# Optimization experiments

Measured on AMD Instinct MI355X. Metric: run time of the kernel, lower is better.

Reference implementation:

```python
import jax, jax.numpy as jnp
import numpy as np

NUM_HIGH = 3
CHANNELS = 3

def _gauss_kernel(channels):
    k = jnp.array([[1., 4., 6., 4., 1.],
                   [4., 16., 24., 16., 4.],
                   [6., 24., 36., 24., 6.],
                   [4., 16., 24., 16., 4.],
                   [1., 4., 6., 4., 1.]], dtype=jnp.float32) / 256.0
    # depthwise kernel layout OIHW with I=1, O=channels
    return jnp.broadcast_to(k, (channels, 1, 5, 5))

def conv_gauss(img, kernel):
    # reflect-pad by 2 on H,W then depthwise (grouped) 5x5 conv, VALID
    p = jnp.pad(img, ((0, 0), (0, 0), (2, 2), (2, 2)), mode='reflect')
    return jax.lax.conv_general_dilated(
        p, kernel, window_strides=(1, 1), padding='VALID',
        feature_group_count=img.shape[1],
        dimension_numbers=('NCHW', 'OIHW', 'NCHW'))

def downsample(x):
    return x[:, :, ::2, ::2]

def upsample(x, kernel):
    B, C, H, W = x.shape
    x_up = jnp.zeros((B, C, 2 * H, 2 * W), dtype=x.dtype).at[:, :, ::2, ::2].set(x)
    return conv_gauss(x_up, 4.0 * kernel)

def setup_inputs() -> dict:
    key = jax.random.key(0)
    img = jax.random.normal(key, (8, CHANNELS, 1024, 1024), dtype=jnp.float32)
    kernel = _gauss_kernel(CHANNELS)
    return {"img": img, "kernel": kernel}

def reference(img, kernel):
    # pyramid_decom: Laplacian pyramid (H,W divisible by 2**NUM_HIGH, so no interpolate)
    current = img
    pyr = []
    for _ in range(NUM_HIGH):
        filtered = conv_gauss(current, kernel)
        down = downsample(filtered)
        up = upsample(down, kernel)
        pyr.append(current - up)
        current = down
    pyr.append(current)
    return tuple(pyr)
```

## Files before the change

### kernel.cpp

```cpp
#include <hip/hip_runtime.h>


__device__ __forceinline__ int refl(int t, int n) {
    if (t < 0) t = -t;
    if (t >= n) t = 2 * (n - 1) - t;
    return t;
}

__global__ __launch_bounds__(256, 6) void lap_scan_kernel(
    const float* __restrict__ cur, float* __restrict__ lap,
    float* __restrict__ down, int H, int W, int sh)
{
    const int wid = threadIdx.x >> 6, lane = threadIdx.x & 63;
    const int x0 = blockIdx.x * 128;
    const int y0 = (blockIdx.y * 4 + wid) * sh;
    const int img = blockIdx.z;
    const int Hh = H >> 1, Wh = W >> 1;

    const float* curb = cur + (size_t)img * H * W;
    float* lapb = lap + (size_t)img * H * W;
    float* downb = down + (size_t)img * Hh * Wh;

    const int c0 = x0 + 2 * lane;
    const bool haloLane = (lane < 2) | (lane >= 62);
    const int hc0 = (lane < 2) ? (x0 - 4 + 2 * lane) : (x0 + 4 + 2 * lane);
    const bool xb = (x0 == 0) || (x0 + 128 == W);
    const int hg0 = refl(hc0, W), hg1 = refl(hc0 + 1, W);

    auto loadOwn = [&](int rho) -> float2 {
        return *(const float2*)(curb + (size_t)refl(y0 + rho, H) * W + c0);
    };
    auto loadHalo = [&](int rho) -> float2 {
        const float* rp = curb + (size_t)refl(y0 + rho, H) * W;
        float2 v;
        if (xb) { v.x = rp[hg0]; v.y = rp[hg1]; }
        else    { v = *(const float2*)(rp + hc0); }
        return v;
    };

    float2 w0 = loadOwn(-4), w1 = loadOwn(-3), w2 = loadOwn(-2),
           w3 = loadOwn(-1), w4 = loadOwn(0);
    float2 h0 = {0,0}, h1 = {0,0}, h2 = {0,0}, h3 = {0,0}, h4 = {0,0};
    if (haloLane) {
        h0 = loadHalo(-4); h1 = loadHalo(-3); h2 = loadHalo(-2);
        h3 = loadHalo(-1); h4 = loadHalo(0);
    }

    float dm2a = 0, dm2b = 0, dm2c = 0, dm1a = 0, dm1b = 0, dm1c = 0;
    const int aEnd = sh >> 1;

    for (int a = -1; a <= aEnd; ++a) {
        float2 nw3 = {0,0}, nw4 = {0,0}, nh3 = {0,0}, nh4 = {0,0};
        const bool more = (a < aEnd);
        if (more) {
            nw3 = loadOwn(2 * a + 3); nw4 = loadOwn(2 * a + 4);
            if (haloLane) { nh3 = loadHalo(2 * a + 3); nh4 = loadHalo(2 * a + 4); }
        }

        float vE = w0.x + 4.f * w1.x + 6.f * w2.x + 4.f * w3.x + w4.x;
        float vO = w0.y + 4.f * w1.y + 6.f * w2.y + 4.f * w3.y + w4.y;
        float hE = h0.x + 4.f * h1.x + 6.f * h2.x + 4.f * h3.x + h4.x;
        float hO = h0.y + 4.f * h1.y + 6.f * h2.y + 4.f * h3.y + h4.y;

        float bhE0 = __shfl(hE, 0),  bhO0 = __shfl(hO, 0);
        float bhE1 = __shfl(hE, 1),  bhO1 = __shfl(hO, 1);
        float bhE62 = __shfl(hE, 62), bhO62 = __shfl(hO, 62);
        float bhE63 = __shfl(hE, 63);
        float bvE0 = __shfl(vE, 0);
        float bvE63 = __shfl(vE, 63), bvO63 = __shfl(vO, 63);

        float sE = __shfl_up(vE, 1), sO = __shfl_up(vO, 1);
        float nE = __shfl_down(vE, 1);
        float eL = (lane == 0) ? bhE1 : sE;
        float oL = (lane == 0) ? bhO1 : sO;
        float eR = (lane == 63) ? bhE62 : nE;

        float dv = (eL + 4.f * oL + 6.f * vE + 4.f * vO + eR) * (1.f / 256.f);
        float dvm1 = (bhE0 + 4.f * bhO0 + 6.f * bhE1 + 4.f * bhO1 + bvE0) * (1.f / 256.f);
        float dvp64 = (bvE63 + 4.f * bvO63 + 6.f * bhE62 + 4.f * bhO62 + bhE63) * (1.f / 256.f);

        float su = __shfl_up(dv, 1), sd = __shfl_down(dv, 1);
        float da = (lane == 0) ? dvm1 : su;
        float db = dv;
        float dc = (lane == 63) ? dvp64 : sd;

        if (a >= 0 && a < aEnd)
            downb[(size_t)((y0 >> 1) + a) * Wh + (x0 >> 1) + lane] = dv;

        if (a >= 1) {
            float CEa = dm2a + 6.f * dm1a + da;
            float CEb = dm2b + 6.f * dm1b + db;
            float CEc = dm2c + 6.f * dm1c + dc;
            float COa = 4.f * (dm1a + da);
            float COb = 4.f * (dm1b + db);
            float COc = 4.f * (dm1c + dc);
            float2 oe, oo;
            oe.x = w0.x - (CEa + 6.f * CEb + CEc) * (1.f / 64.f);
            oe.y = w0.y - 4.f * (CEb + CEc) * (1.f / 64.f);
            oo.x = w1.x - (COa + 6.f * COb + COc) * (1.f / 64.f);
            oo.y = w1.y - 4.f * (COb + COc) * (1.f / 64.f);
            *(float2*)(lapb + (size_t)(y0 + 2 * a - 2) * W + c0) = oe;
            *(float2*)(lapb + (size_t)(y0 + 2 * a - 1) * W + c0) = oo;
        }

        dm2a = dm1a; dm2b = dm1b; dm2c = dm1c;
        dm1a = da;   dm1b = db;   dm1c = dc;
        w0 = w2; w1 = w3; w2 = w4;
        if (more) { w3 = nw3; w4 = nw4; }
        h0 = h2; h1 = h3; h2 = h4;
        if (more) { h3 = nh3; h4 = nh4; }
    }
}

extern "C" void kernel_launch(void* const* d_in, const int* in_sizes, int n_in,
                              void* d_out, int out_size, void* d_ws, size_t ws_size,
                              hipStream_t stream) {
    const float* img = (const float*)d_in[0];
    float* out = (float*)d_out;

    const long long BC = 8LL * 3;
    const long long n0 = BC * 1024 * 1024;
    const long long n1 = BC * 512 * 512;
    const long long n2 = BC * 256 * 256;

    float* out0 = out;
    float* out1 = out0 + n0;
    float* out2 = out1 + n1;
    float* out3 = out2 + n2;

    float* ws0 = (float*)d_ws;
    float* ws1 = ws0 + n1;

    lap_scan_kernel<<<dim3(1024 / 128, 1024 / (4 * 32), (int)BC), 256, 0, stream>>>(
        img, out0, ws0, 1024, 1024, 32);
    lap_scan_kernel<<<dim3(512 / 128, 512 / (4 * 16), (int)BC), 256, 0, stream>>>(
        ws0, out1, ws1, 512, 512, 16);
    lap_scan_kernel<<<dim3(256 / 128, 256 / (4 * 8), (int)BC), 256, 0, stream>>>(
        ws1, out2, out3, 256, 256, 8);
}
```

Before: 71.80 us.

## Widen per-lane tile to four columns with float4 loads and fewer halo shuffles

Each lane now processes four input columns (256 per wave) using float4 loads and stores, and two downsampled outputs per row, so the cross-lane work shrinks to a few neighbour shuffles with single halo lanes at each edge. The aim is fewer memory instructions per byte and less shuffle and broadcast overhead per output. Strip heights for the smaller pyramid levels are halved to keep the block count up, and launch bounds are relaxed to allow more registers. In exchange, register pressure and halo reloads per strip increase, and occupancy may drop.

Result: slower. 99.76 us (+38.9%).

```diff
diff --git a/kernel.cpp b/kernel.cpp
--- a/kernel.cpp
+++ b/kernel.cpp
@@ -7,12 +7,12 @@
     return t;
 }
 
-__global__ __launch_bounds__(256, 6) void lap_scan_kernel(
+__global__ __launch_bounds__(256, 5) void lap_scan_kernel(
     const float* __restrict__ cur, float* __restrict__ lap,
     float* __restrict__ down, int H, int W, int sh)
 {
     const int wid = threadIdx.x >> 6, lane = threadIdx.x & 63;
-    const int x0 = blockIdx.x * 128;
+    const int x0 = blockIdx.x * 256;
     const int y0 = (blockIdx.y * 4 + wid) * sh;
     const int img = blockIdx.z;
     const int Hh = H >> 1, Wh = W >> 1;
@@ -21,94 +21,102 @@
     float* lapb = lap + (size_t)img * H * W;
     float* downb = down + (size_t)img * Hh * Wh;
 
-    const int c0 = x0 + 2 * lane;
-    const bool haloLane = (lane < 2) | (lane >= 62);
-    const int hc0 = (lane < 2) ? (x0 - 4 + 2 * lane) : (x0 + 4 + 2 * lane);
-    const bool xb = (x0 == 0) || (x0 + 128 == W);
-    const int hg0 = refl(hc0, W), hg1 = refl(hc0 + 1, W);
+    const int c0 = x0 + 4 * lane;
+    const bool haloLane = (lane == 0) | (lane == 63);
+    const int hc0 = (lane == 0) ? (x0 - 4) : (x0 + 256);
+    const bool xb = (x0 == 0) || (x0 + 256 == W);
+    int hg0 = refl(hc0, W), hg1 = refl(hc0 + 1, W),
+        hg2 = refl(hc0 + 2, W), hg3 = refl(hc0 + 3, W);
 
-    auto loadOwn = [&](int rho) -> float2 {
-        return *(const float2*)(curb + (size_t)refl(y0 + rho, H) * W + c0);
+    auto loadOwn = [&](int rho) -> float4 {
+        return *(const float4*)(curb + (size_t)refl(y0 + rho, H) * W + c0);
     };
-    auto loadHalo = [&](int rho) -> float2 {
+    auto loadHalo = [&](int rho) -> float4 {
         const float* rp = curb + (size_t)refl(y0 + rho, H) * W;
-        float2 v;
-        if (xb) { v.x = rp[hg0]; v.y = rp[hg1]; }
-        else    { v = *(const float2*)(rp + hc0); }
+        float4 v;
+        if (xb) { v.x = rp[hg0]; v.y = rp[hg1]; v.z = rp[hg2]; v.w = rp[hg3]; }
+        else    { v = *(const float4*)(rp + hc0); }
         return v;
     };
 
-    float2 w0 = loadOwn(-4), w1 = loadOwn(-3), w2 = loadOwn(-2),
+    float4 w0 = loadOwn(-4), w1 = loadOwn(-3), w2 = loadOwn(-2),
            w3 = loadOwn(-1), w4 = loadOwn(0);
-    float2 h0 = {0,0}, h1 = {0,0}, h2 = {0,0}, h3 = {0,0}, h4 = {0,0};
+    float4 z4 = {0.f, 0.f, 0.f, 0.f};
+    float4 h0 = z4, h1 = z4, h2 = z4, h3 = z4, h4 = z4;
     if (haloLane) {
         h0 = loadHalo(-4); h1 = loadHalo(-3); h2 = loadHalo(-2);
         h3 = loadHalo(-1); h4 = loadHalo(0);
     }
 
-    float dm2a = 0, dm2b = 0, dm2c = 0, dm1a = 0, dm1b = 0, dm1c = 0;
+    float qm20 = 0, qm21 = 0, qm22 = 0, qm23 = 0;
+    float qm10 = 0, qm11 = 0, qm12 = 0, qm13 = 0;
     const int aEnd = sh >> 1;
 
     for (int a = -1; a <= aEnd; ++a) {
-        float2 nw3 = {0,0}, nw4 = {0,0}, nh3 = {0,0}, nh4 = {0,0};
+        float4 nw3 = z4, nw4 = z4, nh3 = z4, nh4 = z4;
         const bool more = (a < aEnd);
         if (more) {
             nw3 = loadOwn(2 * a + 3); nw4 = loadOwn(2 * a + 4);
             if (haloLane) { nh3 = loadHalo(2 * a + 3); nh4 = loadHalo(2 * a + 4); }
         }
 
-        float vE = w0.x + 4.f * w1.x + 6.f * w2.x + 4.f * w3.x + w4.x;
-        float vO = w0.y + 4.f * w1.y + 6.f * w2.y + 4.f * w3.y + w4.y;
-        float hE = h0.x + 4.f * h1.x + 6.f * h2.x + 4.f * h3.x + h4.x;
-        float hO = h0.y + 4.f * h1.y + 6.f * h2.y + 4.f * h3.y + h4.y;
+        float vE0 = w0.x + 4.f * w1.x + 6.f * w2.x + 4.f * w3.x + w4.x;
+        float vO0 = w0.y + 4.f * w1.y + 6.f * w2.y + 4.f * w3.y + w4.y;
+        float vE1 = w0.z + 4.f * w1.z + 6.f * w2.z + 4.f * w3.z + w4.z;
+        float vO1 = w0.w + 4.f * w1.w + 6.f * w2.w + 4.f * w3.w + w4.w;
+        float hE0 = h0.x + 4.f * h1.x + 6.f * h2.x + 4.f * h3.x + h4.x;
+        float hO0 = h0.y + 4.f * h1.y + 6.f * h2.y + 4.f * h3.y + h4.y;
+        float hE1 = h0.z + 4.f * h1.z + 6.f * h2.z + 4.f * h3.z + h4.z;
+        float hO1 = h0.w + 4.f * h1.w + 6.f * h2.w + 4.f * h3.w + h4.w;
 
-        float bhE0 = __shfl(hE, 0),  bhO0 = __shfl(hO, 0);
-        float bhE1 = __shfl(hE, 1),  bhO1 = __shfl(hO, 1);
-        float bhE62 = __shfl(hE, 62), bhO62 = __shfl(hO, 62);
-        float bhE63 = __shfl(hE, 63);
-        float bvE0 = __shfl(vE, 0);
-        float bvE63 = __shfl(vE, 63), bvO63 = __shfl(vO, 63);
+        float pE1 = __shfl_up(vE1, 1);
+        float pO1 = __shfl_up(vO1, 1);
+        float nE0 = __shfl_down(vE0, 1);
+        if (lane == 0)  { pE1 = hE1; pO1 = hO1; }
+        if (lane == 63) { nE0 = hE0; }
+        float d0 = (pE1 + 4.f * pO1 + 6.f * vE0 + 4.f * vO0 + vE1) * (1.f / 256.f);
+        float d1 = (vE0 + 4.f * vO0 + 6.f * vE1 + 4.f * vO1 + nE0) * (1.f / 256.f);
 
-        float sE = __shfl_up(vE, 1), sO = __shfl_up(vO, 1);
-        float nE = __shfl_down(vE, 1);
-        float eL = (lane == 0) ? bhE1 : sE;
-        float oL = (lane == 0) ? bhO1 : sO;
-        float eR = (lane == 63) ? bhE62 : nE;
+        float q0 = __shfl_up(d1, 1);
+        float q3 = __shfl_down(d0, 1);
+        if (lane == 0)
+            q0 = (hE0 + 4.f * hO0 + 6.f * hE1 + 4.f * hO1 + vE0) * (1.f / 256.f);
+        if (lane == 63)
+            q3 = (vE1 + 4.f * vO1 + 6.f * hE0 + 4.f * hO0 + hE1) * (1.f / 256.f);
+        float q1 = d0, q2 = d1;
 
-        float dv = (eL + 4.f * oL + 6.f * vE + 4.f * vO + eR) * (1.f / 256.f);
-        float dvm1 = (bhE0 + 4.f * bhO0 + 6.f * bhE1 + 4.f * bhO1 + bvE0) * (1.f / 256.f);
-        float dvp64 = (bvE63 + 4.f * bvO63 + 6.f * bhE62 + 4.f * bhO62 + bhE63) * (1.f / 256.f);
-
-        float su = __shfl_up(dv, 1), sd = __shfl_down(dv, 1);
-        float da = (lane == 0) ? dvm1 : su;
-        float db = dv;
-        float dc = (lane == 63) ? dvp64 : sd;
-
-        if (a >= 0 && a < aEnd)
-            downb[(size_t)((y0 >> 1) + a) * Wh + (x0 >> 1) + lane] = dv;
+        if (a >= 0 && a < aEnd) {
+            float2 dd; dd.x = d0; dd.y = d1;
+            *(float2*)(downb + (size_t)((y0 >> 1) + a) * Wh + (x0 >> 1) + 2 * lane) = dd;
+        }
 
         if (a >= 1) {
-            float CEa = dm2a + 6.f * dm1a + da;
-            float CEb = dm2b + 6.f * dm1b + db;
-            float CEc = dm2c + 6.f * dm1c + dc;
-            float COa = 4.f * (dm1a + da);
-            float COb = 4.f * (dm1b + db);
-            float COc = 4.f * (dm1c + dc);
-            float2 oe, oo;
-            oe.x = w0.x - (CEa + 6.f * CEb + CEc) * (1.f / 64.f);
-            oe.y = w0.y - 4.f * (CEb + CEc) * (1.f / 64.f);
-            oo.x = w1.x - (COa + 6.f * COb + COc) * (1.f / 64.f);
-            oo.y = w1.y - 4.f * (COb + COc) * (1.f / 64.f);
-            *(float2*)(lapb + (size_t)(y0 + 2 * a - 2) * W + c0) = oe;
-            *(float2*)(lapb + (size_t)(y0 + 2 * a - 1) * W + c0) = oo;
+            float CE0 = qm20 + 6.f * qm10 + q0;
+            float CE1 = qm21 + 6.f * qm11 + q1;
+            float CE2 = qm22 + 6.f * qm12 + q2;
+            float CE3 = qm23 + 6.f * qm13 + q3;
+            float CO0 = 4.f * (qm10 + q0);
+            float CO1 = 4.f * (qm11 + q1);
+            float CO2 = 4.f * (qm12 + q2);
+            float CO3 = 4.f * (qm13 + q3);
+            float4 oe, oo;
+            oe.x = w0.x - (CE0 + 6.f * CE1 + CE2) * (1.f / 64.f);
+            oe.y = w0.y - 4.f * (CE1 + CE2) * (1.f / 64.f);
+            oe.z = w0.z - (CE1 + 6.f * CE2 + CE3) * (1.f / 64.f);
+            oe.w = w0.w - 4.f * (CE2 + CE3) * (1.f / 64.f);
+            oo.x = w1.x - (CO0 + 6.f * CO1 + CO2) * (1.f / 64.f);
+            oo.y = w1.y - 4.f * (CO1 + CO2) * (1.f / 64.f);
+            oo.z = w1.z - (CO1 + 6.f * CO2 + CO3) * (1.f / 64.f);
+            oo.w = w1.w - 4.f * (CO2 + CO3) * (1.f / 64.f);
+            *(float4*)(lapb + (size_t)(y0 + 2 * a - 2) * W + c0) = oe;
+            *(float4*)(lapb + (size_t)(y0 + 2 * a - 1) * W + c0) = oo;
         }
 
-        dm2a = dm1a; dm2b = dm1b; dm2c = dm1c;
-        dm1a = da;   dm1b = db;   dm1c = dc;
+        qm20 = qm10; qm21 = qm11; qm22 = qm12; qm23 = qm13;
+        qm10 = q0;   qm11 = q1;   qm12 = q2;   qm13 = q3;
         w0 = w2; w1 = w3; w2 = w4;
-        if (more) { w3 = nw3; w4 = nw4; }
         h0 = h2; h1 = h3; h2 = h4;
-        if (more) { h3 = nh3; h4 = nh4; }
+        if (more) { w3 = nw3; w4 = nw4; h3 = nh3; h4 = nh4; }
     }
 }
 
@@ -131,10 +139,10 @@
     float* ws0 = (float*)d_ws;
     float* ws1 = ws0 + n1;
 
-    lap_scan_kernel<<<dim3(1024 / 128, 1024 / (4 * 32), (int)BC), 256, 0, stream>>>(
+    lap_scan_kernel<<<dim3(1024 / 256, 1024 / (4 * 32), (int)BC), 256, 0, stream>>>(
         img, out0, ws0, 1024, 1024, 32);
-    lap_scan_kernel<<<dim3(512 / 128, 512 / (4 * 16), (int)BC), 256, 0, stream>>>(
-        ws0, out1, ws1, 512, 512, 16);
-    lap_scan_kernel<<<dim3(256 / 128, 256 / (4 * 8), (int)BC), 256, 0, stream>>>(
-        ws1, out2, out3, 256, 256, 8);
+    lap_scan_kernel<<<dim3(512 / 256, 512 / (4 * 8), (int)BC), 256, 0, stream>>>(
+        ws0, out1, ws1, 512, 512, 8);
+    lap_scan_kernel<<<dim3(256 / 256, 256 / (4 * 4), (int)BC), 256, 0, stream>>>(
+        ws1, out2, out3, 256, 256, 4);
 }
```
